# Performance work log

Hardware: AMD Instinct MI355X
Metric: run time of the kernel (lower is better)

Reference implementation:

```python
import jax, jax.numpy as jnp
import numpy as np

EPS = 1e-6


def _conv(x, w, b=None, pad=0, groups=1):
    out = jax.lax.conv_general_dilated(
        x, w, window_strides=(1, 1), padding=[(pad, pad), (pad, pad)],
        feature_group_count=groups,
        dimension_numbers=("NCHW", "OIHW", "NCHW"))
    if b is not None:
        out = out + b[None, :, None, None]
    return out


def _win_patches(t):
    # t: [B, C, H, W] -> [B, C, 25, H, W]; 5x5 zero-padded sliding windows
    # (equivalent to torch nn.Unfold(5, padding=2), grouped per channel)
    B, C, H, W = t.shape
    p = jax.lax.conv_general_dilated_patches(
        t.reshape(B * C, 1, H, W), filter_shape=(5, 5),
        window_strides=(1, 1), padding=[(2, 2), (2, 2)])
    return p.reshape(B, C, 25, H, W)


def _gradient_consistency(gx, gy):
    mag = jnp.sqrt(gx * gx + gy * gy + EPS)
    direction = jnp.arctan2(gy, gx)
    dp = _win_patches(direction)          # [B,C,25,H,W]
    mp = _win_patches(mag)                # [B,C,25,H,W]
    sum_m = mp.sum(axis=2)                # [B,C,H,W]
    wmean = (dp * mp).sum(axis=2) / (sum_m + EPS)
    wvar = ((dp - wmean[:, :, None]) ** 2 * mp).sum(axis=2) / (sum_m + EPS)
    wstd = jnp.sqrt(wvar)
    return 1.0 - jnp.tanh(wstd)           # [B,C,H,W]


def setup_inputs() -> dict:
    key = jax.random.key(0)
    B, C, H, W = 2, 64, 128, 128
    C4 = C // 4
    ks = jax.random.split(key, 12)
    s = 0.02
    sobel_x = jnp.array([[-1, 0, 1], [-2, 0, 2], [-1, 0, 1]], jnp.float32)
    sobel_y = jnp.array([[-1, -2, -1], [0, 0, 0], [1, 2, 1]], jnp.float32)
    return {
        "x": jax.random.normal(ks[0], (B, C, H, W), jnp.float32),
        "w_gx": jnp.tile(sobel_x[None, None], (C, 1, 1, 1)),
        "w_gy": jnp.tile(sobel_y[None, None], (C, 1, 1, 1)),
        "ga_w1": jax.random.normal(ks[1], (C, 2 * C, 1, 1), jnp.float32) * s,
        "ga_b1": jnp.zeros((C,), jnp.float32),
        "ga_w2": jax.random.normal(ks[2], (C4, C, 1, 1), jnp.float32) * s,
        "ga_b2": jnp.zeros((C4,), jnp.float32),
        "cd_w1": jax.random.normal(ks[3], (C4, C4, 3, 3), jnp.float32) * s,
        "cd_b1": jnp.zeros((C4,), jnp.float32),
        "cd_w2": jax.random.normal(ks[4], (1, C4, 1, 1), jnp.float32) * s,
        "cd_b2": jnp.zeros((1,), jnp.float32),
        "ec_w1": jax.random.normal(ks[5], (C, C, 3, 3), jnp.float32) * s,
        "ec_b1": jnp.zeros((C,), jnp.float32),
        "ec_w2": jax.random.normal(ks[6], (C, C, 3, 3), jnp.float32) * s,
        "ec_b2": jnp.zeros((C,), jnp.float32),
        "alpha": jnp.float32(0.1),
    }


def reference(x, w_gx, w_gy, ga_w1, ga_b1, ga_w2, ga_b2,
              cd_w1, cd_b1, cd_w2, cd_b2,
              ec_w1, ec_b1, ec_w2, ec_b2, alpha):
    C = x.shape[1]
    # Sobel depthwise gradients
    gx = _conv(x, w_gx, pad=1, groups=C)
    gy = _conv(x, w_gy, pad=1, groups=C)
    # gradient analyzer (1x1 convs)
    gf = jnp.concatenate([gx, gy], axis=1)
    ga = jax.nn.relu(_conv(gf, ga_w1, ga_b1))
    ga = jax.nn.relu(_conv(ga, ga_w2, ga_b2))
    # windowed weighted direction stats
    consistency = _gradient_consistency(gx, gy)
    # consistency detector
    ew = jax.nn.relu(_conv(ga, cd_w1, cd_b1, pad=1))
    ew = jax.nn.sigmoid(_conv(ew, cd_w2, cd_b2))        # [B,1,H,W]
    ew = ew * consistency.mean(axis=1, keepdims=True)
    # edge branch
    ee = jax.nn.relu(_conv(x, ec_w1, ec_b1, pad=1))
    ee = _conv(ee, ec_w2, ec_b2, pad=1)
    return x + alpha * ew * ee
```

## Files before the change

### kernel.cpp

```cpp
#include <hip/hip_runtime.h>
#include <math.h>

#define Hd 128
#define Wd 128
#define HW 16384
#define EPSc 1e-6f

typedef __attribute__((ext_vector_type(8))) short s8v;
typedef __attribute__((ext_vector_type(4))) float f4v;

__device__ __forceinline__ unsigned short f2bf(float f) {
    unsigned int u = __float_as_uint(f);
    unsigned int r = (u + 0x7FFFu + ((u >> 16) & 1u)) >> 16;
    return (unsigned short)r;
}

__device__ __forceinline__ float rcpf(float x) { return __builtin_amdgcn_rcpf(x); }

__device__ __forceinline__ float fatan2(float sy, float sx) {
    float ax = fabsf(sx), ay = fabsf(sy);
    float mx = fmaxf(ax, ay), mn = fminf(ax, ay);
    float q = mn * rcpf(mx);
    float s = q * q;
    float r = q * fmaf(s, fmaf(s, fmaf(s, fmaf(s, 0.0208351f, -0.0851330f),
                                       0.1801410f), -0.3302995f), 0.9998660f);
    if (ay > ax) r = 1.5707963268f - r;
    if (sx < 0.f) r = 3.14159265359f - r;
    r = (sy < 0.f) ? -r : r;
    return (mx == 0.f) ? 0.f : r;
}

__global__ __launch_bounds__(256, 8)
void k_A(const float* __restrict__ x,
         const float* __restrict__ wgx, const float* __restrict__ wgy,
         const float* __restrict__ ga_w1, const float* __restrict__ ga_w2,
         const float* __restrict__ cd_w1,
         const float* __restrict__ ec_w1, const float* __restrict__ ec_w2,
         unsigned short* __restrict__ gxgyh, float* __restrict__ cmPart,
         unsigned short* __restrict__ xh,
         unsigned short* __restrict__ w1m, unsigned short* __restrict__ w2m,
         float* __restrict__ cd_w1t,
         unsigned short* __restrict__ w1h, unsigned short* __restrict__ w2h) {
    __shared__ float xt[484];
    __shared__ float lm[480];
    __shared__ float ld[480];
    int bid = blockIdx.x;
    int tid = threadIdx.x;

    if (bid < 2048) {
        int bx = bid & 7, by = (bid >> 3) & 7, z = bid >> 6;
        int tx = tid & 15, ty = tid >> 4;
        int x0 = bx * 16, y0 = by * 16;
        int b = z >> 4, cb = (z & 15) * 4;
        float acc = 0.f;
        for (int c = 0; c < 4; c++) {
            int ch = cb + c;
            const float* xp = x + (size_t)(b * 64 + ch) * HW;
            float wx[9], wy[9];
#pragma unroll
            for (int i = 0; i < 9; i++) { wx[i] = wgx[ch * 9 + i]; wy[i] = wgy[ch * 9 + i]; }
            __syncthreads();
            for (int i = tid; i < 484; i += 256) {
                int yy = i / 22, xx = i - yy * 22;
                int gyy = y0 - 3 + yy, gxx = x0 - 3 + xx;
                xt[i] = (gyy >= 0 && gyy < Hd && gxx >= 0 && gxx < Wd) ? xp[gyy * Wd + gxx] : 0.f;
            }
            __syncthreads();
            for (int i = tid; i < 400; i += 256) {
                int yy = i / 20, xx = i - yy * 20;
                int gyy = y0 - 2 + yy, gxx = x0 - 2 + xx;
                float m = 0.f, d = 0.f, sx = 0.f, sy = 0.f;
                if (gyy >= 0 && gyy < Hd && gxx >= 0 && gxx < Wd) {
#pragma unroll
                    for (int dy = 0; dy < 3; dy++)
#pragma unroll
                        for (int dx = 0; dx < 3; dx++) {
                            float v = xt[(yy + dy) * 22 + xx + dx];
                            sx = fmaf(wx[dy * 3 + dx], v, sx);
                            sy = fmaf(wy[dy * 3 + dx], v, sy);
                        }
                    m = sqrtf(sx * sx + sy * sy + EPSc);
                    d = fatan2(sy, sx);
                }
                lm[yy * 24 + xx] = m;
                ld[yy * 24 + xx] = d;
                if (yy >= 2 && yy < 18 && xx >= 2 && xx < 18) {
                    size_t pb = ((size_t)b * HW + gyy * Wd + gxx) * 128;
                    gxgyh[pb + ch] = f2bf(sx);
                    gxgyh[pb + 64 + ch] = f2bf(sy);
                }
            }
            __syncthreads();
            float mv[25], dv[25];
            float sm = 0.f, sdm = 0.f;
#pragma unroll
            for (int r = 0; r < 5; r++)
#pragma unroll
                for (int cx = 0; cx < 5; cx++) {
                    int idx = (ty + r) * 24 + tx + cx;
                    float m = lm[idx], d = ld[idx];
                    mv[r * 5 + cx] = m;
                    dv[r * 5 + cx] = d;
                    sm += m;
                    sdm = fmaf(d, m, sdm);
                }
            float rinv = rcpf(sm + EPSc);
            float wmean = sdm * rinv;
            float sv = 0.f;
#pragma unroll
            for (int t = 0; t < 25; t++) { float dd = dv[t] - wmean; sv = fmaf(dd * dd, mv[t], sv); }
            float wstd = sqrtf(sv * rinv);
            acc += 2.f * rcpf(__expf(2.f * wstd) + 1.f);
        }
        cmPart[(size_t)z * HW + (y0 + ty) * Wd + x0 + tx] = acc * (1.f / 64.f);
        return;
    }
    if (bid < 2560) {
        int idx = (bid - 2048) * 256 + tid;
        int cg = idx >> 15;
        int p  = idx & 32767;
        int b = p >> 14, s = p & (HW - 1);
        const float* xp = x + ((size_t)b * 64 + cg * 16) * HW + s;
        alignas(16) unsigned short buf[16];
#pragma unroll
        for (int k = 0; k < 16; k++) buf[k] = f2bf(xp[k * HW]);
        uint4* dst = (uint4*)(xh + (size_t)p * 64 + cg * 16);
        dst[0] = ((const uint4*)buf)[0];
        dst[1] = ((const uint4*)buf)[1];
        return;
    }
    int i = (bid - 2560) * 256 + tid;
    if (i < 36864) {
        int t = i >> 12, co = (i >> 6) & 63, ci = i & 63;
        w1h[i] = f2bf(ec_w1[(co * 64 + ci) * 9 + t]);
    } else if (i < 73728) {
        int j = i - 36864;
        int t = j >> 12, co = (j >> 6) & 63, ci = j & 63;
        w2h[j] = f2bf(ec_w2[(co * 64 + ci) * 9 + t]);
    } else if (i < 81920) {
        int j = i - 73728;
        w1m[j] = f2bf(ga_w1[j]);
    } else if (i < 82944) {
        int j = i - 81920;
        w2m[j] = f2bf(ga_w2[j]);
    } else if (i < 85248) {
        int j = i - 82944;
        int co = j & 15, r = j >> 4, t = r % 9, ci = r / 9;
        cd_w1t[j] = cd_w1[(co * 16 + ci) * 9 + t];
    }
}

__global__ __launch_bounds__(256, 2)
void k_B(const unsigned short* __restrict__ xh,
         const unsigned short* __restrict__ w1h, const float* __restrict__ ec_b1,
         unsigned short* __restrict__ ee1h,
         const unsigned short* __restrict__ gxgyh,
         const unsigned short* __restrict__ w1m, const float* __restrict__ b1,
         const unsigned short* __restrict__ w2m, const float* __restrict__ b2,
         float* __restrict__ ga2) {
    __shared__ unsigned short shb[12288];
    int bid = blockIdx.x;
    int tid = threadIdx.x;
    int lane = tid & 63, wv = tid >> 6;
    int l15 = lane & 15, lq = lane >> 4;

    if (bid < 512) {
        unsigned short* tile = shb;
        int j = bid;
        int x0 = (j & 15) * 8, y0 = ((j >> 4) & 15) * 8;
        int b = j >> 8;
        const size_t ibase = (size_t)b * HW * 64;

        for (int i = tid; i < 800; i += 256) {
            int py = i / 80;
            int r = i - py * 80;
            int px = r >> 3, cg = r & 7;
            int gy = y0 - 1 + py, gx = x0 - 1 + px;
            uint4 v = {0u, 0u, 0u, 0u};
            if (gy >= 0 && gy < Hd && gx >= 0 && gx < Wd)
                v = *(const uint4*)(xh + ibase + (size_t)(gy * Wd + gx) * 64 + cg * 8);
            int rowlin = py * 10 + px;
            int scg = cg ^ (rowlin & 7);
            *(uint4*)(tile + rowlin * 64 + scg * 8) = v;
        }
        int co_base = wv * 16;
        s8v af[9][2];
#pragma unroll
        for (int t = 0; t < 9; t++)
#pragma unroll
            for (int h = 0; h < 2; h++)
                af[t][h] = *(const s8v*)(w1h + ((t * 64 + co_base + l15) * 64 + h * 32 + lq * 8));
        f4v bv = *(const f4v*)(ec_b1 + co_base + lq * 4);
        f4v acc[4];
#pragma unroll
        for (int n = 0; n < 4; n++) acc[n] = bv;
        __syncthreads();
#pragma unroll
        for (int n = 0; n < 4; n++) {
            int px = n * 16 + l15;
            int pyy = px >> 3, pxx = px & 7;
#pragma unroll
            for (int dy = 0; dy < 3; dy++) {
#pragma unroll
                for (int dx = 0; dx < 3; dx++) {
                    int rowlin = (pyy + dy) * 10 + (pxx + dx);
                    int sw = rowlin & 7;
                    const unsigned short* tp = tile + rowlin * 64;
                    s8v b0 = *(const s8v*)(tp + (lq ^ sw) * 8);
                    s8v b1v = *(const s8v*)(tp + ((4 + lq) ^ sw) * 8);
                    int t = dy * 3 + dx;
                    acc[n] = __builtin_amdgcn_mfma_f32_16x16x32_bf16(af[t][0], b0, acc[n], 0, 0, 0);
                    acc[n] = __builtin_amdgcn_mfma_f32_16x16x32_bf16(af[t][1], b1v, acc[n], 0, 0, 0);
                }
            }
        }
#pragma unroll
        for (int n = 0; n < 4; n++) {
            int px = n * 16 + l15;
            int sp = (y0 + (px >> 3)) * Wd + x0 + (px & 7);
            alignas(8) unsigned short pk[4];
#pragma unroll
            for (int r = 0; r < 4; r++) pk[r] = f2bf(fmaxf(acc[n][r], 0.f));
            *(uint2*)(ee1h + ibase + (size_t)sp * 64 + co_base + lq * 4) = *(const uint2*)pk;
        }
        return;
    }

    unsigned short* la = shb;
    unsigned short* lp = shb + 8192;
    int p0 = (bid - 512) * 64;
    int b = p0 >> 14;
    int s0 = p0 & (HW - 1);

    const unsigned short* src = gxgyh + (size_t)p0 * 128;
    for (int i = tid; i < 1024; i += 256) {
        int px = i >> 4, cg = i & 15;
        uint4 v = *(const uint4*)(src + px * 128 + cg * 8);
        *(uint4*)(la + px * 128 + ((cg ^ (px & 15)) * 8)) = v;
    }
    int co_base = wv * 16;
    s8v af[4];
#pragma unroll
    for (int h = 0; h < 4; h++)
        af[h] = *(const s8v*)(w1m + (co_base + l15) * 128 + h * 32 + lq * 8);
    f4v bv = *(const f4v*)(b1 + co_base + lq * 4);
    f4v acc[4];
#pragma unroll
    for (int n = 0; n < 4; n++) acc[n] = bv;
    __syncthreads();
#pragma unroll
    for (int n = 0; n < 4; n++) {
        const unsigned short* tp = la + (n * 16 + l15) * 128;
#pragma unroll
        for (int h = 0; h < 4; h++) {
            s8v bb = *(const s8v*)(tp + (((h * 4 + lq) ^ l15) * 8));
            acc[n] = __builtin_amdgcn_mfma_f32_16x16x32_bf16(af[h], bb, acc[n], 0, 0, 0);
        }
    }
    int co = co_base + lq * 4;
    int og = co >> 3;
#pragma unroll
    for (int n = 0; n < 4; n++) {
        int px = n * 16 + l15;
        alignas(8) unsigned short pk[4];
#pragma unroll
        for (int r = 0; r < 4; r++) pk[r] = f2bf(fmaxf(acc[n][r], 0.f));
        *(uint2*)(lp + px * 64 + ((og ^ (px & 7)) * 8) + (co & 7)) = *(const uint2*)pk;
    }
    __syncthreads();
    s8v af2[2];
#pragma unroll
    for (int h = 0; h < 2; h++)
        af2[h] = *(const s8v*)(w2m + l15 * 64 + h * 32 + lq * 8);
    f4v acc2 = *(const f4v*)(b2 + lq * 4);
    int px2 = wv * 16 + l15;
    const unsigned short* tp2 = lp + px2 * 64;
#pragma unroll
    for (int h = 0; h < 2; h++) {
        s8v bb = *(const s8v*)(tp2 + (((h * 4 + lq) ^ (px2 & 7)) * 8));
        acc2 = __builtin_amdgcn_mfma_f32_16x16x32_bf16(af2[h], bb, acc2, 0, 0, 0);
    }
    float* op = ga2 + (size_t)b * 16 * HW + s0 + px2;
#pragma unroll
    for (int r = 0; r < 4; r++)
        op[(lq * 4 + r) * HW] = fmaxf(acc2[r], 0.f);
}

__global__ __launch_bounds__(256, 4)
void k_cd1ew(const float* __restrict__ ga2, const float* __restrict__ w1t,
             const float* __restrict__ b1, const float* __restrict__ w2,
             const float* __restrict__ b2, const float* __restrict__ cmPart,
             float* __restrict__ ew) {
    __shared__ float lds[16][324];
    int tid = threadIdx.x;
    int tx = tid & 15, ty = tid >> 4;
    int x0 = blockIdx.x * 16, y0 = blockIdx.y * 16;
    int b = blockIdx.z;
    const float* ip = ga2 + (size_t)b * 16 * HW;
    float acc[16];
#pragma unroll
    for (int co = 0; co < 16; co++) acc[co] = b1[co];
#pragma unroll
    for (int ci = 0; ci < 16; ci++) {
        const float* sp = ip + ci * HW;
        for (int i = tid; i < 324; i += 256) {
            int yy = i / 18, xx = i - yy * 18;
            int gy = y0 - 1 + yy, gx = x0 - 1 + xx;
            lds[ci][i] = (gy >= 0 && gy < Hd && gx >= 0 && gx < Wd) ? sp[gy * Wd + gx] : 0.f;
        }
    }
    __syncthreads();
    for (int ci = 0; ci < 16; ci++) {
        const float* wp = w1t + ci * 9 * 16;
        float pv[9];
#pragma unroll
        for (int r = 0; r < 3; r++)
#pragma unroll
            for (int cx = 0; cx < 3; cx++)
                pv[r * 3 + cx] = lds[ci][(ty + r) * 18 + tx + cx];
#pragma unroll
        for (int t = 0; t < 9; t++)
#pragma unroll
            for (int co = 0; co < 16; co++)
                acc[co] = fmaf(pv[t], wp[t * 16 + co], acc[co]);
    }
    float e = b2[0];
#pragma unroll
    for (int co = 0; co < 16; co++) e = fmaf(fmaxf(acc[co], 0.f), w2[co], e);
    float sig = rcpf(1.f + __expf(-e));
    int sp = (y0 + ty) * Wd + x0 + tx;
    float cmv = 0.f;
#pragma unroll
    for (int q = 0; q < 16; q++) cmv += cmPart[(size_t)((b << 4) + q) * HW + sp];
    ew[b * HW + sp] = sig * cmv;
}

__global__ __launch_bounds__(256, 2)
void k_conv64f(const unsigned short* __restrict__ inh,
               const unsigned short* __restrict__ wh,
               const float* __restrict__ bias,
               float* __restrict__ outf,
               const float* __restrict__ x,
               const float* __restrict__ ew,
               const float* __restrict__ alpha_p) {
    __shared__ unsigned short tile[100 * 64];
    int tid = threadIdx.x;
    int x0 = blockIdx.x * 8, y0 = blockIdx.y * 8;
    int b = blockIdx.z;
    const size_t ibase = (size_t)b * HW * 64;

    for (int i = tid; i < 800; i += 256) {
        int py = i / 80;
        int r = i - py * 80;
        int px = r >> 3, cg = r & 7;
        int gy = y0 - 1 + py, gx = x0 - 1 + px;
        uint4 v = {0u, 0u, 0u, 0u};
        if (gy >= 0 && gy < Hd && gx >= 0 && gx < Wd)
            v = *(const uint4*)(inh + ibase + (size_t)(gy * Wd + gx) * 64 + cg * 8);
        int rowlin = py * 10 + px;
        int scg = cg ^ (rowlin & 7);
        *(uint4*)(tile + rowlin * 64 + scg * 8) = v;
    }
    int lane = tid & 63;
    int wv = tid >> 6;
    int l15 = lane & 15, lq = lane >> 4;
    int co_base = wv * 16;
    s8v af[9][2];
#pragma unroll
    for (int t = 0; t < 9; t++)
#pragma unroll
        for (int h = 0; h < 2; h++)
            af[t][h] = *(const s8v*)(wh + ((t * 64 + co_base + l15) * 64 + h * 32 + lq * 8));
    f4v bv = *(const f4v*)(bias + co_base + lq * 4);
    f4v acc[4];
#pragma unroll
    for (int n = 0; n < 4; n++) acc[n] = bv;
    __syncthreads();
#pragma unroll
    for (int n = 0; n < 4; n++) {
        int px = n * 16 + l15;
        int pyy = px >> 3, pxx = px & 7;
#pragma unroll
        for (int dy = 0; dy < 3; dy++) {
#pragma unroll
            for (int dx = 0; dx < 3; dx++) {
                int rowlin = (pyy + dy) * 10 + (pxx + dx);
                int sw = rowlin & 7;
                const unsigned short* tp = tile + rowlin * 64;
                s8v b0 = *(const s8v*)(tp + (lq ^ sw) * 8);
                s8v b1v = *(const s8v*)(tp + ((4 + lq) ^ sw) * 8);
                int t = dy * 3 + dx;
                acc[n] = __builtin_amdgcn_mfma_f32_16x16x32_bf16(af[t][0], b0, acc[n], 0, 0, 0);
                acc[n] = __builtin_amdgcn_mfma_f32_16x16x32_bf16(af[t][1], b1v, acc[n], 0, 0, 0);
            }
        }
    }
#pragma unroll
    for (int n = 0; n < 4; n++) {
        int px = n * 16 + l15;
        int sp = (y0 + (px >> 3)) * Wd + x0 + (px & 7);
        float ae = alpha_p[0] * ew[b * HW + sp];
#pragma unroll
        for (int r = 0; r < 4; r++) {
            size_t o = (size_t)(b * 64 + co_base + lq * 4 + r) * HW + sp;
            outf[o] = fmaf(ae, acc[n][r], x[o]);
        }
    }
}

extern "C" void kernel_launch(void* const* d_in, const int* in_sizes, int n_in,
                              void* d_out, int out_size, void* d_ws, size_t ws_size,
                              hipStream_t stream) {
    const float* x     = (const float*)d_in[0];
    const float* wgx   = (const float*)d_in[1];
    const float* wgy   = (const float*)d_in[2];
    const float* ga_w1 = (const float*)d_in[3];
    const float* ga_b1 = (const float*)d_in[4];
    const float* ga_w2 = (const float*)d_in[5];
    const float* ga_b2 = (const float*)d_in[6];
    const float* cd_w1 = (const float*)d_in[7];
    const float* cd_b1 = (const float*)d_in[8];
    const float* cd_w2 = (const float*)d_in[9];
    const float* cd_b2 = (const float*)d_in[10];
    const float* ec_w1 = (const float*)d_in[11];
    const float* ec_b1 = (const float*)d_in[12];
    const float* ec_w2 = (const float*)d_in[13];
    const float* ec_b2 = (const float*)d_in[14];
    const float* alpha = (const float*)d_in[15];
    float* out = (float*)d_out;
    float* ws  = (float*)d_ws;

    const size_t N = 2 * 64 * HW;

    unsigned short* gxgyh = (unsigned short*)ws;
    float* ga2    = ws + N;
    float* cmPart = ga2 + 2 * 16 * HW;
    float* ew     = cmPart + 32 * HW;
    float* cd_w1t = ew + 2 * HW;
    unsigned short* w1h = (unsigned short*)(cd_w1t + 2304);
    unsigned short* w2h = w1h + 36864;
    unsigned short* w1m = w2h + 36864;
    unsigned short* w2m = w1m + 8192;
    unsigned short* xh   = (unsigned short*)(ws + 2 * N);
    unsigned short* ee1h = xh + N;

    k_A<<<2893, 256, 0, stream>>>(x, wgx, wgy, ga_w1, ga_w2, cd_w1, ec_w1, ec_w2,
                                  gxgyh, cmPart, xh, w1m, w2m, cd_w1t, w1h, w2h);
    k_B<<<1024, 256, 0, stream>>>(xh, w1h, ec_b1, ee1h,
                                  gxgyh, w1m, ga_b1, w2m, ga_b2, ga2);
    k_cd1ew<<<dim3(8, 8, 2), 256, 0, stream>>>(ga2, cd_w1t, cd_b1, cd_w2, cd_b2,
                                               cmPart, ew);
    k_conv64f<<<dim3(16, 16, 2), 256, 0, stream>>>(ee1h, w2h, ec_b2, out, x, ew, alpha);
}
```

Before: 158.0 us.

## Fuse consistency-detector conv and edge weight into final edge conv kernel

Removes the separate k_cd1ew launch and computes the cd 3x3 conv, sigmoid and consistency-mean product inside the final conv kernel. Each 8x8 tile loads a 10x10x16 halo of ga2 into LDS, and each lane computes 4 of the 16 output channels, reduced with cross-lane shuffles. The ew intermediate buffer and its global round trip go away, and one kernel launch is saved. In exchange, the halo recompute adds redundant work, along with extra LDS use and a second barrier in the MFMA kernel.

```diff
diff --git a/kernel.cpp b/kernel.cpp
--- a/kernel.cpp
+++ b/kernel.cpp
@@ -286,64 +286,20 @@
         op[(lq * 4 + r) * HW] = fmaxf(acc2[r], 0.f);
 }
 
-__global__ __launch_bounds__(256, 4)
-void k_cd1ew(const float* __restrict__ ga2, const float* __restrict__ w1t,
-             const float* __restrict__ b1, const float* __restrict__ w2,
-             const float* __restrict__ b2, const float* __restrict__ cmPart,
-             float* __restrict__ ew) {
-    __shared__ float lds[16][324];
-    int tid = threadIdx.x;
-    int tx = tid & 15, ty = tid >> 4;
-    int x0 = blockIdx.x * 16, y0 = blockIdx.y * 16;
-    int b = blockIdx.z;
-    const float* ip = ga2 + (size_t)b * 16 * HW;
-    float acc[16];
-#pragma unroll
-    for (int co = 0; co < 16; co++) acc[co] = b1[co];
-#pragma unroll
-    for (int ci = 0; ci < 16; ci++) {
-        const float* sp = ip + ci * HW;
-        for (int i = tid; i < 324; i += 256) {
-            int yy = i / 18, xx = i - yy * 18;
-            int gy = y0 - 1 + yy, gx = x0 - 1 + xx;
-            lds[ci][i] = (gy >= 0 && gy < Hd && gx >= 0 && gx < Wd) ? sp[gy * Wd + gx] : 0.f;
-        }
-    }
-    __syncthreads();
-    for (int ci = 0; ci < 16; ci++) {
-        const float* wp = w1t + ci * 9 * 16;
-        float pv[9];
-#pragma unroll
-        for (int r = 0; r < 3; r++)
-#pragma unroll
-            for (int cx = 0; cx < 3; cx++)
-                pv[r * 3 + cx] = lds[ci][(ty + r) * 18 + tx + cx];
-#pragma unroll
-        for (int t = 0; t < 9; t++)
-#pragma unroll
-            for (int co = 0; co < 16; co++)
-                acc[co] = fmaf(pv[t], wp[t * 16 + co], acc[co]);
-    }
-    float e = b2[0];
-#pragma unroll
-    for (int co = 0; co < 16; co++) e = fmaf(fmaxf(acc[co], 0.f), w2[co], e);
-    float sig = rcpf(1.f + __expf(-e));
-    int sp = (y0 + ty) * Wd + x0 + tx;
-    float cmv = 0.f;
-#pragma unroll
-    for (int q = 0; q < 16; q++) cmv += cmPart[(size_t)((b << 4) + q) * HW + sp];
-    ew[b * HW + sp] = sig * cmv;
-}
-
 __global__ __launch_bounds__(256, 2)
-void k_conv64f(const unsigned short* __restrict__ inh,
-               const unsigned short* __restrict__ wh,
-               const float* __restrict__ bias,
-               float* __restrict__ outf,
-               const float* __restrict__ x,
-               const float* __restrict__ ew,
-               const float* __restrict__ alpha_p) {
+void k_CD(const unsigned short* __restrict__ inh,
+          const unsigned short* __restrict__ wh,
+          const float* __restrict__ bias,
+          const float* __restrict__ ga2,
+          const float* __restrict__ cd_w1t, const float* __restrict__ cd_b1,
+          const float* __restrict__ cd_w2, const float* __restrict__ cd_b2,
+          const float* __restrict__ cmPart,
+          float* __restrict__ outf,
+          const float* __restrict__ x,
+          const float* __restrict__ alpha_p) {
     __shared__ unsigned short tile[100 * 64];
+    __shared__ float lg[100 * 17];
+    __shared__ float lew[64];
     int tid = threadIdx.x;
     int x0 = blockIdx.x * 8, y0 = blockIdx.y * 8;
     int b = blockIdx.z;
@@ -361,6 +317,16 @@
         int scg = cg ^ (rowlin & 7);
         *(uint4*)(tile + rowlin * 64 + scg * 8) = v;
     }
+    for (int i = tid; i < 1600; i += 256) {
+        int ci = i / 100;
+        int r = i - ci * 100;
+        int yy = r / 10, xx = r - yy * 10;
+        int gy = y0 - 1 + yy, gx = x0 - 1 + xx;
+        float v = (gy >= 0 && gy < Hd && gx >= 0 && gx < Wd)
+                      ? ga2[((size_t)b * 16 + ci) * HW + gy * Wd + gx] : 0.f;
+        lg[r * 17 + ci] = v;
+    }
+
     int lane = tid & 63;
     int wv = tid >> 6;
     int l15 = lane & 15, lq = lane >> 4;
@@ -376,6 +342,46 @@
 #pragma unroll
     for (int n = 0; n < 4; n++) acc[n] = bv;
     __syncthreads();
+
+    {
+        int pxl = wv * 16 + l15;
+        int py = pxl >> 3, pxx = pxl & 7;
+        float ae0 = cd_b1[lq * 4 + 0], ae1 = cd_b1[lq * 4 + 1];
+        float ae2 = cd_b1[lq * 4 + 2], ae3 = cd_b1[lq * 4 + 3];
+        for (int ci = 0; ci < 16; ci++) {
+            float pv[9];
+#pragma unroll
+            for (int dy = 0; dy < 3; dy++)
+#pragma unroll
+                for (int dx = 0; dx < 3; dx++)
+                    pv[dy * 3 + dx] = lg[((py + dy) * 10 + pxx + dx) * 17 + ci];
+            const float* wp = cd_w1t + ci * 144 + lq * 4;
+#pragma unroll
+            for (int t = 0; t < 9; t++) {
+                ae0 = fmaf(pv[t], wp[t * 16 + 0], ae0);
+                ae1 = fmaf(pv[t], wp[t * 16 + 1], ae1);
+                ae2 = fmaf(pv[t], wp[t * 16 + 2], ae2);
+                ae3 = fmaf(pv[t], wp[t * 16 + 3], ae3);
+            }
+        }
+        float ep = fmaxf(ae0, 0.f) * cd_w2[lq * 4 + 0]
+                 + fmaxf(ae1, 0.f) * cd_w2[lq * 4 + 1]
+                 + fmaxf(ae2, 0.f) * cd_w2[lq * 4 + 2]
+                 + fmaxf(ae3, 0.f) * cd_w2[lq * 4 + 3];
+        int sp = (y0 + py) * Wd + x0 + pxx;
+        float cp = 0.f;
+#pragma unroll
+        for (int q = 0; q < 4; q++)
+            cp += cmPart[(size_t)((b << 4) + lq * 4 + q) * HW + sp];
+        ep += __shfl_xor(ep, 16);
+        ep += __shfl_xor(ep, 32);
+        cp += __shfl_xor(cp, 16);
+        cp += __shfl_xor(cp, 32);
+        float sig = rcpf(1.f + __expf(-(cd_b2[0] + ep)));
+        if (lane < 16) lew[wv * 16 + lane] = sig * cp;
+    }
+    __syncthreads();
+
 #pragma unroll
     for (int n = 0; n < 4; n++) {
         int px = n * 16 + l15;
@@ -395,11 +401,12 @@
             }
         }
     }
+    float alp = alpha_p[0];
 #pragma unroll
     for (int n = 0; n < 4; n++) {
         int px = n * 16 + l15;
         int sp = (y0 + (px >> 3)) * Wd + x0 + (px & 7);
-        float ae = alpha_p[0] * ew[b * HW + sp];
+        float ae = alp * lew[px];
 #pragma unroll
         for (int r = 0; r < 4; r++) {
             size_t o = (size_t)(b * 64 + co_base + lq * 4 + r) * HW + sp;
@@ -435,8 +442,7 @@
     unsigned short* gxgyh = (unsigned short*)ws;
     float* ga2    = ws + N;
     float* cmPart = ga2 + 2 * 16 * HW;
-    float* ew     = cmPart + 32 * HW;
-    float* cd_w1t = ew + 2 * HW;
+    float* cd_w1t = cmPart + 32 * HW;
     unsigned short* w1h = (unsigned short*)(cd_w1t + 2304);
     unsigned short* w2h = w1h + 36864;
     unsigned short* w1m = w2h + 36864;
@@ -448,7 +454,7 @@
                                   gxgyh, cmPart, xh, w1m, w2m, cd_w1t, w1h, w2h);
     k_B<<<1024, 256, 0, stream>>>(xh, w1h, ec_b1, ee1h,
                                   gxgyh, w1m, ga_b1, w2m, ga_b2, ga2);
-    k_cd1ew<<<dim3(8, 8, 2), 256, 0, stream>>>(ga2, cd_w1t, cd_b1, cd_w2, cd_b2,
-                                               cmPart, ew);
-    k_conv64f<<<dim3(16, 16, 2), 256, 0, stream>>>(ee1h, w2h, ec_b2, out, x, ew, alpha);
-}
+    k_CD<<<dim3(16, 16, 2), 256, 0, stream>>>(ee1h, w2h, ec_b2, ga2,
+                                              cd_w1t, cd_b1, cd_w2, cd_b2,
+                                              cmPart, out, x, alpha);
+}
```

Measured after the change: 150.7 us. -4.6%, faster.
